# Kernel tuning notes

Measured on AMD Instinct MI355X. Metric: run time of the kernel, lower is better.

## Reference

```python
import jax, jax.numpy as jnp
import numpy as np

# Module dims (match init_kwargs / input_specs)
V = 25        # number of graph nodes (chain skeleton)
K = 3         # max receptive-field size (neighbors incl. self), padded
CIN = 64
COUT = 64
N = 16
T = 512
TK = 3        # temporal_kernel
PAD = TK // 2 # time_pad default


def _build_graph():
    # Chain adjacency with self-links: node i <-> {i-1, i, i+1}
    A = np.zeros((V, V), np.float32)
    for i in range(V):
        A[i, i] = 1.0
        if i > 0:
            A[i, i - 1] = 1.0
        if i < V - 1:
            A[i, i + 1] = 1.0
    # Pad each node's neighbor list to K entries; mask marks real neighbors.
    idx = np.zeros((V, K), np.int32)
    mask = np.zeros((V, K), bool)
    for i in range(V):
        nb = np.where(A[i] != 0)[0]
        idx[i, : len(nb)] = nb
        mask[i, : len(nb)] = True
    return idx, mask


def setup_inputs() -> dict:
    key = jax.random.key(0)
    k_x, k_w, k_b = jax.random.split(key, 3)
    x = jax.random.normal(k_x, (N, CIN, V, T), dtype=jnp.float32)
    # One Conv2d kernel per node: [V, C_out, C_in, K, TK]; padded neighbor
    # slots are zeroed via mask inside reference().
    W = jax.random.normal(k_w, (V, COUT, CIN, K, TK), dtype=jnp.float32) * 0.05
    b = jax.random.normal(k_b, (V, COUT), dtype=jnp.float32) * 0.05
    idx_np, mask_np = _build_graph()
    return {
        "x": x,
        "W": W,
        "b": b,
        "idx": jnp.asarray(idx_np),
        "mask": jnp.asarray(mask_np),
    }


def reference(x, W, b, idx, mask):
    # x: [N, C, V, T]; W: [V, O, C, K, TK]; b: [V, O]; idx/mask: [V, K]
    Tt = x.shape[-1]
    # Zero out padded neighbor slots so padded rows contribute nothing
    # (equivalent to torch's variable-height per-node kernels).
    Wm = jnp.where(mask[:, None, None, :, None], W, 0.0)
    # Temporal zero padding (Conv2d padding=(0, time_pad))
    xp = jnp.pad(x, ((0, 0), (0, 0), (0, 0), (PAD, PAD)))
    # Batched neighbor gather: [N, C, V, K, T + 2*PAD]
    g = xp[:, :, idx, :]
    # Cross-correlation over the TK temporal taps (stride 1)
    out = jnp.zeros((x.shape[0], W.shape[1], V, Tt), dtype=x.dtype)
    for kt in range(TK):
        out = out + jnp.einsum(
            "ncvkt,vock->novt", g[..., kt : kt + Tt], Wm[..., kt]
        )
    out = out + b.T[None, :, :, None]  # per-node bias [O, V]
    return out
```

## Files before the change

kernel.cpp:

```cpp
#include <hip/hip_runtime.h>
#include <hip/hip_bf16.h>

#define NB   16
#define CINC 64
#define COUTC 64
#define NV   25
#define TLEN 512
#define KK   3
#define TKK  3

typedef short short8 __attribute__((ext_vector_type(8)));
typedef float f32x4  __attribute__((ext_vector_type(4)));
typedef float f32x16 __attribute__((ext_vector_type(16)));

#define XT_ROWS 514
#define XS_STRIDE 17408
#define NWT3BLK (NV * 9)

__device__ __forceinline__ unsigned pack_bf16(float lo, float hi) {
  __hip_bfloat16 l = __float2bfloat16(lo);
  __hip_bfloat16 h = __float2bfloat16(hi);
  unsigned short ul = *reinterpret_cast<unsigned short*>(&l);
  unsigned short uh = *reinterpret_cast<unsigned short*>(&h);
  return (unsigned)ul | ((unsigned)uh << 16);
}

__global__ __launch_bounds__(256) void prep_all(
    const float* __restrict__ x, const float* __restrict__ W,
    const unsigned char* __restrict__ mask_raw,
    __hip_bfloat16* __restrict__ Wt3, __hip_bfloat16* __restrict__ xT) {
  __shared__ float ts[64][65];
  int bid = blockIdx.x;
  if (bid < NWT3BLK) {
    int blk = bid;
    int v = blk / 9, kkt = blk % 9, k = kkt / 3, kt = kkt % 3;
    const int* mi = (const int*)mask_raw;
    int ok = 1;
    for (int i = 0; i < 18; ++i) {
      int m = mi[i];
      if (m != 0 && m != 1) ok = 0;
    }
    int m = ok ? mi[v * KK + k] : (int)(mask_raw[v * KK + k] != 0);
    const float* Wv = W + (size_t)v * COUTC * CINC * 9;
    __hip_bfloat16* dst = Wt3 + (size_t)blk * 4096;
    for (int i = threadIdx.x; i < 4096; i += 256) {
      int e     = i & 7;
      int lane  = (i >> 3) & 63;
      int ks    = (i >> 9) & 3;
      int oslab = i >> 11;
      int o = oslab * 32 + (lane & 31);
      int c = ks * 16 + 8 * (lane >> 5) + e;
      float val = m ? Wv[(o * CINC + c) * 9 + k * 3 + kt] : 0.f;
      dst[i] = __float2bfloat16(val);
    }
    return;
  }
  bid -= NWT3BLK;
  const int tb = (bid & 7) * 64;
  const int vn = bid >> 3;
  const int v  = vn % NV;
  const int n  = vn / NV;
  const int tid = threadIdx.x;
  for (int i = tid; i < 1024; i += 256) {
    int c = i >> 4, tq = (i & 15) * 4;
    float4 val = *(const float4*)(x + (((size_t)n * CINC + c) * NV + v) * TLEN + tb + tq);
    ts[c][tq + 0] = val.x;
    ts[c][tq + 1] = val.y;
    ts[c][tq + 2] = val.z;
    ts[c][tq + 3] = val.w;
  }
  __syncthreads();
  unsigned* base = (unsigned*)(xT + ((size_t)(n * NV + v) * XT_ROWS) * CINC);
  for (int i = tid; i < 512; i += 256) {
    int c8 = i & 7, t = i >> 3;
    int c0 = c8 * 8;
    uint4 d;
    d.x = pack_bf16(ts[c0 + 0][t], ts[c0 + 1][t]);
    d.y = pack_bf16(ts[c0 + 2][t], ts[c0 + 3][t]);
    d.z = pack_bf16(ts[c0 + 4][t], ts[c0 + 5][t]);
    d.w = pack_bf16(ts[c0 + 6][t], ts[c0 + 7][t]);
    *(uint4*)(base + (size_t)(tb + 1 + t) * 32 + c8 * 4) = d;
  }
  if (tb == 0 && tid < 32) base[tid] = 0u;
  if (tb == TLEN - 64 && tid < 32) base[513 * 32 + tid] = 0u;
}

__device__ __forceinline__ const char* slab_base(const __hip_bfloat16* xT,
                                                 int n, int vk, int tb) {
  return (const char*)xT + ((size_t)(n * NV + vk) * XT_ROWS + tb) * 128;
}

__global__ __launch_bounds__(256, 3) void lcn_mfma32(
    const __hip_bfloat16* __restrict__ xT,
    const __hip_bfloat16* __restrict__ Wt3,
    const float* __restrict__ bias,
    const int* __restrict__ idx,
    float* __restrict__ out) {
  __shared__ char xs[KK][XS_STRIDE];
  __shared__ char xs_dummy[1024];

  const int b  = blockIdx.x;
  const int L  = (b & 7) * 200 + (b >> 3);
  const int tb = (L & 3) * 128;
  const int n  = (L >> 2) & 15;
  const int v  = L >> 6;
  const int tid  = threadIdx.x;
  const int lane = tid & 63;
  const int wave = tid >> 6;
  const int os   = wave & 1;
  const int th   = wave >> 1;
  const int hi   = lane >> 5;
  const int l31  = lane & 31;

#define LOAD_A(DST, KIDX)                                                     \
  {                                                                           \
    const short8* wb = (const short8*)Wt3 +                                   \
        ((size_t)((v * KK + (KIDX)) * TKK) * 2 + os) * 256 + lane;            \
    _Pragma("unroll") for (int kt = 0; kt < TKK; ++kt)                        \
      _Pragma("unroll") for (int ks = 0; ks < 4; ++ks)                        \
        DST[kt * 4 + ks] = wb[kt * 512 + (ks << 6)];                          \
  }

#define COMPUTE_K(CB, A)                                                      \
  _Pragma("unroll") for (int kt = 0; kt < TKK; ++kt) {                        \
    {                                                                         \
      const int r  = th * 64 + l31 + kt;                                      \
      const int sw = (r & 7) << 4;                                            \
      const int co = hi * 16;                                                 \
      const char* bp = (CB) + r * 128;                                        \
      _Pragma("unroll") for (int ks = 0; ks < 4; ++ks) {                      \
        short8 bfr = *(const short8*)(bp + ((co + 32 * ks) ^ sw));            \
        acc0 = __builtin_amdgcn_mfma_f32_32x32x16_bf16(A[kt * 4 + ks], bfr,   \
                                                       acc0, 0, 0, 0);        \
      }                                                                       \
    }                                                                         \
    {                                                                         \
      const int r  = th * 64 + 32 + l31 + kt;                                 \
      const int sw = (r & 7) << 4;                                            \
      const int co = hi * 16;                                                 \
      const char* bp = (CB) + r * 128;                                        \
      _Pragma("unroll") for (int ks = 0; ks < 4; ++ks) {                      \
        short8 bfr = *(const short8*)(bp + ((co + 32 * ks) ^ sw));            \
        acc1 = __builtin_amdgcn_mfma_f32_32x32x16_bf16(A[kt * 4 + ks], bfr,   \
                                                       acc1, 0, 0, 0);        \
      }                                                                       \
    }                                                                         \
  }

  short8 aP[12], aQ[12];
  LOAD_A(aP, 0)
  __builtin_amdgcn_sched_barrier(0);
  {
    const char* gb0 = slab_base(xT, n, idx[v * KK + 0], tb);
    const char* gb1 = slab_base(xT, n, idx[v * KK + 1], tb);
    const char* gb2 = slab_base(xT, n, idx[v * KK + 2], tb);
#pragma unroll
    for (int s = 0; s < KK; ++s) {
      const char* gb = (s == 0) ? gb0 : ((s == 1) ? gb1 : gb2);
#pragma unroll
      for (int q = 0; q < 4; ++q) {
        int c = wave + q * 4;
        int Lb = c * 1024 + lane * 16;
        int g = Lb ^ (((Lb >> 7) & 7) << 4);
        __builtin_amdgcn_global_load_lds(
            (const __attribute__((address_space(1))) void*)(gb + g),
            (__attribute__((address_space(3))) void*)(&xs[s][c * 1024]),
            16, 0, 0);
      }
      if (wave == 0) {
        int Lb = 16 * 1024 + lane * 16;
        int g = Lb ^ (((Lb >> 7) & 7) << 4);
        __builtin_amdgcn_global_load_lds(
            (const __attribute__((address_space(1))) void*)(gb + g),
            (__attribute__((address_space(3))) void*)(&xs[s][16 * 1024]),
            16, 0, 0);
      } else {
        __builtin_amdgcn_global_load_lds(
            (const __attribute__((address_space(1))) void*)(gb + lane * 16),
            (__attribute__((address_space(3))) void*)(xs_dummy),
            16, 0, 0);
      }
      __builtin_amdgcn_sched_barrier(0);
    }
  }

  f32x16 acc0 = {}, acc1 = {};

  asm volatile("s_waitcnt vmcnt(10)" ::: "memory");
  __builtin_amdgcn_s_barrier();
  __builtin_amdgcn_sched_barrier(0);
  LOAD_A(aQ, 1)
  COMPUTE_K(xs[0], aP)

  asm volatile("s_waitcnt vmcnt(17)" ::: "memory");
  __builtin_amdgcn_s_barrier();
  __builtin_amdgcn_sched_barrier(0);
  COMPUTE_K(xs[1], aQ)

  asm volatile("s_waitcnt vmcnt(12)" ::: "memory");
  __builtin_amdgcn_s_barrier();
  __builtin_amdgcn_sched_barrier(0);
  LOAD_A(aP, 2)
  COMPUTE_K(xs[2], aP)

#undef LOAD_A
#undef COMPUTE_K

  const float* bv = bias + v * COUTC;
#pragma unroll
  for (int s = 0; s < 2; ++s) {
    const f32x16& acc = s ? acc1 : acc0;
    const int t = tb + th * 64 + s * 32 + l31;
#pragma unroll
    for (int reg = 0; reg < 16; ++reg) {
      int o = os * 32 + 4 * hi + (reg & 3) + 8 * (reg >> 2);
      out[(((size_t)n * COUTC + o) * NV + v) * TLEN + t] = acc[reg] + bv[o];
    }
  }
}

__global__ void prep_mask_kernel(const int* __restrict__ mask_raw,
                                 int* __restrict__ mask_out) {
  __shared__ int fmt;
  if (threadIdx.x == 0) {
    int ok = 1;
    for (int i = 0; i < 18; ++i) {
      int m = mask_raw[i];
      if (m != 0 && m != 1) ok = 0;
    }
    fmt = ok;
  }
  __syncthreads();
  int i = threadIdx.x;
  if (i < NV * KK) {
    int m;
    if (fmt) m = mask_raw[i];
    else     m = (((const unsigned char*)mask_raw)[i] != 0) ? 1 : 0;
    mask_out[i] = m;
  }
}

__global__ void prep_wt_kernel(const float* __restrict__ W,
                               float* __restrict__ Wt) {
  int v   = blockIdx.x / 9;
  int kkt = blockIdx.x % 9;
  const float* Wv = W + (size_t)v * COUTC * CINC * 9;
  float* dst = Wt + (size_t)blockIdx.x * (CINC * COUTC);
  for (int i = threadIdx.x; i < CINC * COUTC; i += 256) {
    int c = i >> 6;
    int o = i & 63;
    dst[i] = Wv[(o * CINC + c) * 9 + kkt];
  }
}

__global__ __launch_bounds__(256, 4) void lcn_main(
    const float* __restrict__ x, const float* __restrict__ Wt,
    const float* __restrict__ b, const int* __restrict__ idx,
    const int* __restrict__ maskn, float* __restrict__ out) {
  __shared__ float xsf[CINC][66];
  __shared__ float wsh[CINC][COUTC];
  const int tb  = blockIdx.x * 64;
  const int v   = blockIdx.y;
  const int n   = blockIdx.z;
  const int tid = threadIdx.x;
  const int t0  = tid & 63;
  const int og  = tid >> 6;
  float acc[16];
#pragma unroll
  for (int j = 0; j < 16; ++j) acc[j] = 0.f;
  for (int k = 0; k < KK; ++k) {
    const int vk = idx[v * KK + k];
    const int mk = maskn[v * KK + k];
    __syncthreads();
    for (int i = tid; i < CINC * 66; i += 256) {
      int c  = i / 66;
      int tt = i - c * 66;
      int gt = tb - 1 + tt;
      float val = 0.f;
      if (mk && gt >= 0 && gt < TLEN)
        val = x[(((size_t)n * CINC + c) * NV + vk) * TLEN + gt];
      xsf[c][tt] = val;
    }
    for (int kt = 0; kt < TKK; ++kt) {
      __syncthreads();
      const float4* src =
          (const float4*)(Wt + ((size_t)(v * KK + k) * TKK + kt) * (CINC * COUTC));
      for (int i = tid; i < CINC * COUTC / 4; i += 256)
        ((float4*)wsh)[i] = src[i];
      __syncthreads();
#pragma unroll 4
      for (int c = 0; c < CINC; ++c) {
        float xv = xsf[c][t0 + kt];
        const float4* wrow = (const float4*)&wsh[c][og * 16];
#pragma unroll
        for (int j4 = 0; j4 < 4; ++j4) {
          float4 wv = wrow[j4];
          acc[j4 * 4 + 0] = fmaf(wv.x, xv, acc[j4 * 4 + 0]);
          acc[j4 * 4 + 1] = fmaf(wv.y, xv, acc[j4 * 4 + 1]);
          acc[j4 * 4 + 2] = fmaf(wv.z, xv, acc[j4 * 4 + 2]);
          acc[j4 * 4 + 3] = fmaf(wv.w, xv, acc[j4 * 4 + 3]);
        }
      }
    }
  }
#pragma unroll
  for (int j = 0; j < 16; ++j) {
    int o = og * 16 + j;
    out[(((size_t)n * COUTC + o) * NV + v) * TLEN + tb + t0] =
        acc[j] + b[v * COUTC + o];
  }
}

extern "C" void kernel_launch(void* const* d_in, const int* in_sizes, int n_in,
                              void* d_out, int out_size, void* d_ws, size_t ws_size,
                              hipStream_t stream) {
  const float* x    = (const float*)d_in[0];
  const float* W    = (const float*)d_in[1];
  const float* b    = (const float*)d_in[2];
  const int*   idx  = (const int*)d_in[3];
  const void*  mask = (const void*)d_in[4];
  float* out = (float*)d_out;

  const size_t WT3_BYTES = (size_t)NV * 9 * 4096 * sizeof(__hip_bfloat16);
  const size_t XT_BYTES  = (size_t)NB * NV * XT_ROWS * CINC * sizeof(__hip_bfloat16);
  const size_t NEED      = 512 + WT3_BYTES + XT_BYTES + 2048;

  if (ws_size >= NEED) {
    __hip_bfloat16* Wt3 = (__hip_bfloat16*)((char*)d_ws + 512);
    __hip_bfloat16* xT  = (__hip_bfloat16*)((char*)d_ws + 512 + WT3_BYTES);
    hipLaunchKernelGGL(prep_all, dim3(NWT3BLK + 8 * NV * NB), dim3(256), 0,
                       stream, x, W, (const unsigned char*)mask, Wt3, xT);
    hipLaunchKernelGGL(lcn_mfma32, dim3(TLEN / 128 * NB * NV), dim3(256), 0,
                       stream, xT, Wt3, b, idx, out);
  } else {
    int*   maskn = (int*)d_ws;
    float* Wt    = (float*)((char*)d_ws + 512);
    hipLaunchKernelGGL(prep_mask_kernel, dim3(1), dim3(128), 0, stream,
                       (const int*)mask, maskn);
    hipLaunchKernelGGL(prep_wt_kernel, dim3(NV * KK * TKK), dim3(256), 0, stream,
                       W, Wt);
    hipLaunchKernelGGL(lcn_main, dim3(TLEN / 64, NV, NB), dim3(256), 0, stream,
                       x, Wt, b, idx, maskn, out);
  }
}
```

Measured before the change: 48.51 us.

## Process two time tiles per block with resident weights and overlapped staging

Each block now handles two consecutive 128-step time tiles instead of one, halving the grid. All 36 weight fragments are loaded into registers once and reused across both tiles. The second tile's LDS staging is issued before the first tile's output stores, so the stores overlap with the loads. Launch bounds drop from 3 to 2 waves-per-EU to make room for the larger register footprint, which lowers occupancy. The block-to-work mapping also changes from the swizzled order to a plain n-fastest order.

```diff
diff --git a/kernel.cpp b/kernel.cpp
--- a/kernel.cpp
+++ b/kernel.cpp
@@ -90,7 +90,7 @@
   return (const char*)xT + ((size_t)(n * NV + vk) * XT_ROWS + tb) * 128;
 }
 
-__global__ __launch_bounds__(256, 3) void lcn_mfma32(
+__global__ __launch_bounds__(256, 2) void lcn_mfma32(
     const __hip_bfloat16* __restrict__ xT,
     const __hip_bfloat16* __restrict__ Wt3,
     const float* __restrict__ bias,
@@ -100,10 +100,9 @@
   __shared__ char xs_dummy[1024];
 
   const int b  = blockIdx.x;
-  const int L  = (b & 7) * 200 + (b >> 3);
-  const int tb = (L & 3) * 128;
-  const int n  = (L >> 2) & 15;
-  const int v  = L >> 6;
+  const int n  = b & 15;
+  const int tc = (b >> 4) & 1;
+  const int v  = b >> 5;
   const int tid  = threadIdx.x;
   const int lane = tid & 63;
   const int wave = tid >> 6;
@@ -112,16 +111,41 @@
   const int hi   = lane >> 5;
   const int l31  = lane & 31;
 
-#define LOAD_A(DST, KIDX)                                                     \
+#define STAGE_PHASE(TBP)                                                      \
   {                                                                           \
-    const short8* wb = (const short8*)Wt3 +                                   \
-        ((size_t)((v * KK + (KIDX)) * TKK) * 2 + os) * 256 + lane;            \
-    _Pragma("unroll") for (int kt = 0; kt < TKK; ++kt)                        \
-      _Pragma("unroll") for (int ks = 0; ks < 4; ++ks)                        \
-        DST[kt * 4 + ks] = wb[kt * 512 + (ks << 6)];                          \
-  }
-
-#define COMPUTE_K(CB, A)                                                      \
+    const char* gbs[KK] = {                                                   \
+        slab_base(xT, n, idx[v * KK + 0], (TBP)),                             \
+        slab_base(xT, n, idx[v * KK + 1], (TBP)),                             \
+        slab_base(xT, n, idx[v * KK + 2], (TBP))};                            \
+    _Pragma("unroll") for (int s = 0; s < KK; ++s) {                          \
+      const char* gb = gbs[s];                                                \
+      _Pragma("unroll") for (int q = 0; q < 4; ++q) {                         \
+        int c = wave + q * 4;                                                 \
+        int Lb = c * 1024 + lane * 16;                                        \
+        int g = Lb ^ (((Lb >> 7) & 7) << 4);                                  \
+        __builtin_amdgcn_global_load_lds(                                     \
+            (const __attribute__((address_space(1))) void*)(gb + g),          \
+            (__attribute__((address_space(3))) void*)(&xs[s][c * 1024]),      \
+            16, 0, 0);                                                        \
+      }                                                                       \
+      if (wave == 0) {                                                        \
+        int Lb = 16 * 1024 + lane * 16;                                       \
+        int g = Lb ^ (((Lb >> 7) & 7) << 4);                                  \
+        __builtin_amdgcn_global_load_lds(                                     \
+            (const __attribute__((address_space(1))) void*)(gb + g),          \
+            (__attribute__((address_space(3))) void*)(&xs[s][16 * 1024]),     \
+            16, 0, 0);                                                        \
+      } else {                                                                \
+        __builtin_amdgcn_global_load_lds(                                     \
+            (const __attribute__((address_space(1))) void*)(gb + lane * 16),  \
+            (__attribute__((address_space(3))) void*)(xs_dummy),              \
+            16, 0, 0);                                                        \
+      }                                                                       \
+      __builtin_amdgcn_sched_barrier(0);                                      \
+    }                                                                         \
+  }
+
+#define COMPUTE_K(CB, KB)                                                     \
   _Pragma("unroll") for (int kt = 0; kt < TKK; ++kt) {                        \
     {                                                                         \
       const int r  = th * 64 + l31 + kt;                                      \
@@ -130,8 +154,8 @@
       const char* bp = (CB) + r * 128;                                        \
       _Pragma("unroll") for (int ks = 0; ks < 4; ++ks) {                      \
         short8 bfr = *(const short8*)(bp + ((co + 32 * ks) ^ sw));            \
-        acc0 = __builtin_amdgcn_mfma_f32_32x32x16_bf16(A[kt * 4 + ks], bfr,   \
-                                                       acc0, 0, 0, 0);        \
+        acc0 = __builtin_amdgcn_mfma_f32_32x32x16_bf16(                       \
+            aA[((KB) + kt) * 4 + ks], bfr, acc0, 0, 0, 0);                    \
       }                                                                       \
     }                                                                         \
     {                                                                         \
@@ -141,82 +165,84 @@
       const char* bp = (CB) + r * 128;                                        \
       _Pragma("unroll") for (int ks = 0; ks < 4; ++ks) {                      \
         short8 bfr = *(const short8*)(bp + ((co + 32 * ks) ^ sw));            \
-        acc1 = __builtin_amdgcn_mfma_f32_32x32x16_bf16(A[kt * 4 + ks], bfr,   \
-                                                       acc1, 0, 0, 0);        \
+        acc1 = __builtin_amdgcn_mfma_f32_32x32x16_bf16(                       \
+            aA[((KB) + kt) * 4 + ks], bfr, acc1, 0, 0, 0);                    \
       }                                                                       \
     }                                                                         \
   }
 
-  short8 aP[12], aQ[12];
-  LOAD_A(aP, 0)
-  __builtin_amdgcn_sched_barrier(0);
+#define STORES(PHB)                                                           \
+  {                                                                           \
+    const float* bv = bias + v * COUTC;                                       \
+    _Pragma("unroll") for (int s = 0; s < 2; ++s) {                           \
+      const f32x16& acc = s ? acc1 : acc0;                                    \
+      const int t = (PHB) + th * 64 + s * 32 + l31;                           \
+      _Pragma("unroll") for (int reg = 0; reg < 16; ++reg) {                  \
+        int o = os * 32 + 4 * hi + (reg & 3) + 8 * (reg >> 2);                \
+        out[(((size_t)n * COUTC + o) * NV + v) * TLEN + t] = acc[reg] + bv[o];\
+      }                                                                       \
+    }                                                                         \
+  }
+
+  short8 aA[36];
   {
-    const char* gb0 = slab_base(xT, n, idx[v * KK + 0], tb);
-    const char* gb1 = slab_base(xT, n, idx[v * KK + 1], tb);
-    const char* gb2 = slab_base(xT, n, idx[v * KK + 2], tb);
-#pragma unroll
-    for (int s = 0; s < KK; ++s) {
-      const char* gb = (s == 0) ? gb0 : ((s == 1) ? gb1 : gb2);
-#pragma unroll
-      for (int q = 0; q < 4; ++q) {
-        int c = wave + q * 4;
-        int Lb = c * 1024 + lane * 16;
-        int g = Lb ^ (((Lb >> 7) & 7) << 4);
-        __builtin_amdgcn_global_load_lds(
-            (const __attribute__((address_space(1))) void*)(gb + g),
-            (__attribute__((address_space(3))) void*)(&xs[s][c * 1024]),
-            16, 0, 0);
-      }
-      if (wave == 0) {
-        int Lb = 16 * 1024 + lane * 16;
-        int g = Lb ^ (((Lb >> 7) & 7) << 4);
-        __builtin_amdgcn_global_load_lds(
-            (const __attribute__((address_space(1))) void*)(gb + g),
-            (__attribute__((address_space(3))) void*)(&xs[s][16 * 1024]),
-            16, 0, 0);
-      } else {
-        __builtin_amdgcn_global_load_lds(
-            (const __attribute__((address_space(1))) void*)(gb + lane * 16),
-            (__attribute__((address_space(3))) void*)(xs_dummy),
-            16, 0, 0);
-      }
-      __builtin_amdgcn_sched_barrier(0);
-    }
-  }
+    const short8* wb = (const short8*)Wt3 + ((size_t)(v * 9) * 2 + os) * 256 + lane;
+#pragma unroll
+    for (int bq = 0; bq < 9; ++bq)
+#pragma unroll
+      for (int ks = 0; ks < 4; ++ks)
+        aA[bq * 4 + ks] = wb[bq * 512 + (ks << 6)];
+  }
+  __builtin_amdgcn_sched_barrier(0);
+  const int tb0 = tc * 256;
+  STAGE_PHASE(tb0)
 
   f32x16 acc0 = {}, acc1 = {};
 
   asm volatile("s_waitcnt vmcnt(10)" ::: "memory");
   __builtin_amdgcn_s_barrier();
   __builtin_amdgcn_sched_barrier(0);
-  LOAD_A(aQ, 1)
-  COMPUTE_K(xs[0], aP)
-
-  asm volatile("s_waitcnt vmcnt(17)" ::: "memory");
-  __builtin_amdgcn_s_barrier();
-  __builtin_amdgcn_sched_barrier(0);
-  COMPUTE_K(xs[1], aQ)
-
-  asm volatile("s_waitcnt vmcnt(12)" ::: "memory");
-  __builtin_amdgcn_s_barrier();
-  __builtin_amdgcn_sched_barrier(0);
-  LOAD_A(aP, 2)
-  COMPUTE_K(xs[2], aP)
-
-#undef LOAD_A
+  COMPUTE_K(xs[0], 0)
+
+  asm volatile("s_waitcnt vmcnt(5)" ::: "memory");
+  __builtin_amdgcn_s_barrier();
+  __builtin_amdgcn_sched_barrier(0);
+  COMPUTE_K(xs[1], 3)
+
+  asm volatile("s_waitcnt vmcnt(0)" ::: "memory");
+  __builtin_amdgcn_s_barrier();
+  __builtin_amdgcn_sched_barrier(0);
+  COMPUTE_K(xs[2], 6)
+
+  __builtin_amdgcn_s_barrier();
+  __builtin_amdgcn_sched_barrier(0);
+  STAGE_PHASE(tb0 + 128)
+  __builtin_amdgcn_sched_barrier(0);
+  STORES(tb0)
+  __builtin_amdgcn_sched_barrier(0);
+  acc0 = (f32x16){};
+  acc1 = (f32x16){};
+
+  asm volatile("s_waitcnt vmcnt(42)" ::: "memory");
+  __builtin_amdgcn_s_barrier();
+  __builtin_amdgcn_sched_barrier(0);
+  COMPUTE_K(xs[0], 0)
+
+  asm volatile("s_waitcnt vmcnt(37)" ::: "memory");
+  __builtin_amdgcn_s_barrier();
+  __builtin_amdgcn_sched_barrier(0);
+  COMPUTE_K(xs[1], 3)
+
+  asm volatile("s_waitcnt vmcnt(32)" ::: "memory");
+  __builtin_amdgcn_s_barrier();
+  __builtin_amdgcn_sched_barrier(0);
+  COMPUTE_K(xs[2], 6)
+
+  STORES(tb0 + 128)
+
+#undef STAGE_PHASE
 #undef COMPUTE_K
-
-  const float* bv = bias + v * COUTC;
-#pragma unroll
-  for (int s = 0; s < 2; ++s) {
-    const f32x16& acc = s ? acc1 : acc0;
-    const int t = tb + th * 64 + s * 32 + l31;
-#pragma unroll
-    for (int reg = 0; reg < 16; ++reg) {
-      int o = os * 32 + 4 * hi + (reg & 3) + 8 * (reg >> 2);
-      out[(((size_t)n * COUTC + o) * NV + v) * TLEN + t] = acc[reg] + bv[o];
-    }
-  }
+#undef STORES
 }
 
 __global__ void prep_mask_kernel(const int* __restrict__ mask_raw,
@@ -330,7 +356,7 @@
     __hip_bfloat16* xT  = (__hip_bfloat16*)((char*)d_ws + 512 + WT3_BYTES);
     hipLaunchKernelGGL(prep_all, dim3(NWT3BLK + 8 * NV * NB), dim3(256), 0,
                        stream, x, W, (const unsigned char*)mask, Wt3, xT);
-    hipLaunchKernelGGL(lcn_mfma32, dim3(TLEN / 128 * NB * NV), dim3(256), 0,
+    hipLaunchKernelGGL(lcn_mfma32, dim3(NB * 2 * NV), dim3(256), 0,
                        stream, xT, Wt3, b, idx, out);
   } else {
     int*   maskn = (int*)d_ws;
```

Result: slower. 56.14 us (+15.7%).
